# Performance work log

Hardware: AMD Instinct MI355X
Metric: run time of the kernel (lower is better)

The kernel has to match this reference:

```python
import jax, jax.numpy as jnp
import numpy as np

HEADS = 4
DIM_HEAD = 32
SCALE = DIM_HEAD ** (-0.5)


def setup_inputs() -> dict:
    key = jax.random.key(0)
    k1, k2, k3, k4 = jax.random.split(key, 4)
    dim = 256
    hidden = HEADS * DIM_HEAD  # 128
    x = jax.random.normal(k1, (8, dim, 48, 48), dtype=jnp.float32)
    w_qkv = jax.random.normal(k2, (3 * hidden, dim), dtype=jnp.float32) * (dim ** -0.5)
    w_out = jax.random.normal(k3, (dim, hidden), dtype=jnp.float32) * (hidden ** -0.5)
    b_out = jax.random.normal(k4, (dim,), dtype=jnp.float32) * 0.01
    return {"x": x, "w_qkv": w_qkv, "w_out": w_out, "b_out": b_out}


def reference(x, w_qkv, w_out, b_out):
    b, c, h, w = x.shape
    n = h * w
    xf = x.reshape(b, c, n)                                  # [b, c, n]
    # 1x1 Conv1d (no bias) == pointwise linear over channels
    qkv = jnp.einsum('oc,bcn->bon', w_qkv, xf)               # [b, 3*hidden, n]
    q, k, v = jnp.split(qkv, 3, axis=1)                      # each [b, hidden, n]
    def to_heads(t):
        return t.reshape(b, HEADS, DIM_HEAD, n)              # b h d n
    q, k, v = to_heads(q) * SCALE, to_heads(k), to_heads(v)
    sim = jnp.einsum('bhdi,bhdj->bhij', q, k)                # [b, h, n, n]
    attn = jax.nn.softmax(sim, axis=-1)                      # stable (max-subtracted)
    out = jnp.einsum('bhij,bhdj->bhid', attn, v)             # [b, h, n, d]
    # 'b h (x y) d -> b (h d) x y'
    out = out.transpose(0, 1, 3, 2).reshape(b, HEADS * DIM_HEAD, n)
    y = jnp.einsum('oc,bcn->bon', w_out, out) + b_out[None, :, None]
    return y.reshape(b, c, h, w)
```

## Files before the change

### kernel.cpp

```cpp
#include <hip/hip_runtime.h>
#include <math.h>

#define NB    8
#define CDIM  256
#define NN    2304
#define NH    4
#define DH    32
#define HIDC  128
#define OC3   384
#define SCALE_LOG2E 0.25503524964550864f
#define SEG   2359296
#define LSEG  73728
#define PPARTS 4
#define JCHUNK 576
#define NITER  18

typedef short  bf16x8 __attribute__((ext_vector_type(8)));
typedef float  f32x4  __attribute__((ext_vector_type(4)));

__device__ __forceinline__ unsigned short f2bf(float f) {
    union { float f; unsigned u; } a; a.f = f;
    unsigned r = a.u + 0x7fffu + ((a.u >> 16) & 1u);
    return (unsigned short)(r >> 16);
}

__device__ __forceinline__ unsigned pack_trunc(float lo, float hi) {
    union { float f; unsigned u; } a, b; a.f = lo; b.f = hi;
    return (b.u & 0xFFFF0000u) | (a.u >> 16);
}

__device__ __forceinline__ float bflo(unsigned u) {
    union { unsigned u; float f; } c; c.u = u << 16; return c.f;
}
__device__ __forceinline__ float bfhi(unsigned u) {
    union { unsigned u; float f; } c; c.u = u & 0xFFFF0000u; return c.f;
}

__global__ __launch_bounds__(256) void qkv_proj_kernel(
    const float* __restrict__ x, const float* __restrict__ w,
    unsigned short* __restrict__ qt, unsigned short* __restrict__ kt,
    unsigned short* __restrict__ vtT)
{
    __shared__ unsigned short As[128 * 40];
    __shared__ unsigned short Bs[128 * 40];
    const int Lb   = (int)blockIdx.x;
    const int xcd  = Lb & 7;
    const int t    = Lb >> 3;
    const int sel  = t % 3;
    const int gl   = t / 3;
    const int group = gl * 8 + xcd;
    const int nb   = group % 18;
    const int b    = group / 18;
    const int n0 = nb * 128;
    const int o0 = sel * 128;

    const int tid  = (int)threadIdx.x;
    const int wave = tid >> 6;
    const int lane = tid & 63;
    const int li   = lane & 15;
    const int g    = lane >> 4;
    const int wm = (wave & 1) * 64;
    const int wn = (wave >> 1) * 64;
    const float* xb = x + (size_t)b * CDIM * NN;

    const int aco = (tid & 7) * 4;
    const int aor = tid >> 3;
    const int n4  = (tid & 31) * 4;
    const int c4  = (tid >> 5) * 4;

    f32x4 acc[4][4];
#pragma unroll
    for (int i = 0; i < 4; ++i)
#pragma unroll
        for (int j = 0; j < 4; ++j) acc[i][j] = (f32x4){0.f, 0.f, 0.f, 0.f};

    float4 wv[4], xv[4];
#pragma unroll
    for (int r = 0; r < 4; ++r)
        wv[r] = *(const float4*)&w[(size_t)(o0 + aor + 32 * r) * CDIM + aco];
#pragma unroll
    for (int dd = 0; dd < 4; ++dd)
        xv[dd] = *(const float4*)&xb[(size_t)(c4 + dd) * NN + n0 + n4];

    for (int k0 = 0; k0 < CDIM; k0 += 32) {
        __syncthreads();
#pragma unroll
        for (int r = 0; r < 4; ++r) {
            uint2 pk;
            pk.x = (unsigned)f2bf(wv[r].x) | ((unsigned)f2bf(wv[r].y) << 16);
            pk.y = (unsigned)f2bf(wv[r].z) | ((unsigned)f2bf(wv[r].w) << 16);
            *(uint2*)&As[(aor + 32 * r) * 40 + aco] = pk;
        }
#pragma unroll
        for (int j = 0; j < 4; ++j) {
            uint2 pk;
            pk.x = (unsigned)f2bf(((const float*)&xv[0])[j])
                 | ((unsigned)f2bf(((const float*)&xv[1])[j]) << 16);
            pk.y = (unsigned)f2bf(((const float*)&xv[2])[j])
                 | ((unsigned)f2bf(((const float*)&xv[3])[j]) << 16);
            *(uint2*)&Bs[(n4 + j) * 40 + c4] = pk;
        }
        __syncthreads();

        const int kn = (k0 + 32 < CDIM) ? (k0 + 32) : k0;
#pragma unroll
        for (int r = 0; r < 4; ++r)
            wv[r] = *(const float4*)&w[(size_t)(o0 + aor + 32 * r) * CDIM + kn + aco];
#pragma unroll
        for (int dd = 0; dd < 4; ++dd)
            xv[dd] = *(const float4*)&xb[(size_t)(kn + c4 + dd) * NN + n0 + n4];

        bf16x8 af[4], bfr[4];
#pragma unroll
        for (int mt = 0; mt < 4; ++mt)
            af[mt] = *(const bf16x8*)&As[(wm + mt * 16 + li) * 40 + g * 8];
#pragma unroll
        for (int nt = 0; nt < 4; ++nt)
            bfr[nt] = *(const bf16x8*)&Bs[(wn + nt * 16 + li) * 40 + g * 8];
#pragma unroll
        for (int mt = 0; mt < 4; ++mt)
#pragma unroll
            for (int nt = 0; nt < 4; ++nt)
                acc[mt][nt] = __builtin_amdgcn_mfma_f32_16x16x32_bf16(
                    af[mt], bfr[nt], acc[mt][nt], 0, 0, 0);
    }

    if (sel < 2) {
        unsigned short* dst = (sel == 0) ? qt : kt;
        const float mul = (sel == 0) ? SCALE_LOG2E : 1.0f;
#pragma unroll
        for (int mt = 0; mt < 4; ++mt) {
            const int ob = o0 + wm + mt * 16 + g * 4;
            const int d0 = ob & 31;
            const int h  = (ob & 127) >> 5;
            const size_t bh = (size_t)(b * NH + h);
#pragma unroll
            for (int nt = 0; nt < 4; ++nt) {
                const int n = n0 + wn + nt * 16 + li;
                const f32x4 a = acc[mt][nt];
                uint2 pk;
                pk.x = (unsigned)f2bf(a[0] * mul) | ((unsigned)f2bf(a[1] * mul) << 16);
                pk.y = (unsigned)f2bf(a[2] * mul) | ((unsigned)f2bf(a[3] * mul) << 16);
                *(uint2*)&dst[(bh * NN + n) * DH + d0] = pk;
            }
        }
    } else {
#pragma unroll
        for (int mt = 0; mt < 4; ++mt) {
            const int ob = o0 + wm + mt * 16 + g * 4;
            const int d0 = ob & 31;
            const int h  = (ob & 127) >> 5;
            const size_t bh = (size_t)(b * NH + h);
#pragma unroll
            for (int nt = 0; nt < 4; ++nt) {
                const int n = n0 + wn + nt * 16 + li;
                const f32x4 a = acc[mt][nt];
#pragma unroll
                for (int r = 0; r < 4; ++r)
                    vtT[(bh * DH + d0 + r) * (size_t)NN + n] = f2bf(a[r]);
            }
        }
    }
}

__global__ __launch_bounds__(256) void attn_kernel(
    const unsigned short* __restrict__ qt, const unsigned short* __restrict__ kt,
    const unsigned short* __restrict__ vtT, unsigned short* __restrict__ Op,
    float* __restrict__ Lp)
{
    __shared__ unsigned short Pl[4][2][16 * 32];
    const int Lb  = (int)blockIdx.x;
    const int xcd = Lb & 7;
    const int t   = Lb >> 3;
    const int ib  = t % 18;
    const int grp = (t / 18) * 8 + xcd;
    const int bh  = grp >> 2;
    const int part = grp & 3;
    const int jbeg = part * JCHUNK;

    const int tid  = (int)threadIdx.x;
    const int wave = tid >> 6;
    const int lane = tid & 63;
    const int li   = lane & 15;
    const int g    = lane >> 4;
    const int i0   = ib * 128 + wave * 32;

    const unsigned short* qb = qt  + (size_t)bh * NN * DH;
    const unsigned short* kb = kt  + (size_t)bh * NN * DH;
    const unsigned short* vb = vtT + (size_t)bh * DH * NN;

    bf16x8 qfA = *(const bf16x8*)(qb + (size_t)(i0 + li) * DH + g * 8);
    bf16x8 qfB = *(const bf16x8*)(qb + (size_t)(i0 + 16 + li) * DH + g * 8);

    bf16x8 ones;
#pragma unroll
    for (int r = 0; r < 8; ++r) ones[r] = (short)0x3F80;

    f32x4 O0A = {0.f,0.f,0.f,0.f}, O1A = {0.f,0.f,0.f,0.f}, LsA = {0.f,0.f,0.f,0.f};
    f32x4 O0B = {0.f,0.f,0.f,0.f}, O1B = {0.f,0.f,0.f,0.f}, LsB = {0.f,0.f,0.f,0.f};
    unsigned short* plA = &Pl[wave][0][0];
    unsigned short* plB = &Pl[wave][1][0];
    const int sw  = li & 6;
    const int pw  = li * 32;
    const int wr0 = pw + ((g ^ sw) << 2);
    const int wr1 = pw + (((4 + g) ^ sw) << 2);
    const int rdo = pw + (((2 * g) ^ sw) << 2);

    const unsigned short* kp0 = kb + (size_t)(jbeg + li) * DH + g * 8;
    const unsigned short* kp1 = kp0 + 16 * DH;
    const unsigned short* vp0 = vb + (size_t)li * NN + jbeg + g * 8;
    const unsigned short* vp1 = vp0 + 16 * NN;

    bf16x8 kf0 = *(const bf16x8*)kp0;
    bf16x8 kf1 = *(const bf16x8*)kp1;
    bf16x8 vf0 = *(const bf16x8*)vp0;
    bf16x8 vf1 = *(const bf16x8*)vp1;

#pragma unroll 2
    for (int it = 0; it < NITER; ++it) {
        f32x4 z = {0.f, 0.f, 0.f, 0.f};
        f32x4 s0A = __builtin_amdgcn_mfma_f32_16x16x32_bf16(kf0, qfA, z, 0, 0, 0);
        f32x4 s0B = __builtin_amdgcn_mfma_f32_16x16x32_bf16(kf0, qfB, z, 0, 0, 0);
        f32x4 s1A = __builtin_amdgcn_mfma_f32_16x16x32_bf16(kf1, qfA, z, 0, 0, 0);
        f32x4 s1B = __builtin_amdgcn_mfma_f32_16x16x32_bf16(kf1, qfB, z, 0, 0, 0);

        kp0 += 32 * DH; kp1 += 32 * DH;
        kf0 = *(const bf16x8*)kp0;
        kf1 = *(const bf16x8*)kp1;

        float p0A[4], p1A[4], p0B[4], p1B[4];
#pragma unroll
        for (int r = 0; r < 4; ++r) {
            p0A[r] = __builtin_amdgcn_exp2f(s0A[r]);
            p1A[r] = __builtin_amdgcn_exp2f(s1A[r]);
            p0B[r] = __builtin_amdgcn_exp2f(s0B[r]);
            p1B[r] = __builtin_amdgcn_exp2f(s1B[r]);
        }

        uint2 wa, wb;
        wa.x = pack_trunc(p0A[0], p0A[1]);  wa.y = pack_trunc(p0A[2], p0A[3]);
        wb.x = pack_trunc(p1A[0], p1A[1]);  wb.y = pack_trunc(p1A[2], p1A[3]);
        *(uint2*)&plA[wr0] = wa;
        *(uint2*)&plA[wr1] = wb;
        wa.x = pack_trunc(p0B[0], p0B[1]);  wa.y = pack_trunc(p0B[2], p0B[3]);
        wb.x = pack_trunc(p1B[0], p1B[1]);  wb.y = pack_trunc(p1B[2], p1B[3]);
        *(uint2*)&plB[wr0] = wa;
        *(uint2*)&plB[wr1] = wb;

        bf16x8 pfA = *(const bf16x8*)&plA[rdo];
        bf16x8 pfB = *(const bf16x8*)&plB[rdo];

        O0A = __builtin_amdgcn_mfma_f32_16x16x32_bf16(vf0,  pfA, O0A, 0, 0, 0);
        O0B = __builtin_amdgcn_mfma_f32_16x16x32_bf16(vf0,  pfB, O0B, 0, 0, 0);
        O1A = __builtin_amdgcn_mfma_f32_16x16x32_bf16(vf1,  pfA, O1A, 0, 0, 0);
        O1B = __builtin_amdgcn_mfma_f32_16x16x32_bf16(vf1,  pfB, O1B, 0, 0, 0);
        LsA = __builtin_amdgcn_mfma_f32_16x16x32_bf16(ones, pfA, LsA, 0, 0, 0);
        LsB = __builtin_amdgcn_mfma_f32_16x16x32_bf16(ones, pfB, LsB, 0, 0, 0);

        vp0 += 32; vp1 += 32;
        vf0 = *(const bf16x8*)vp0;
        vf1 = *(const bf16x8*)vp1;
    }

    unsigned short* obA = Op + (size_t)part * SEG + (size_t)bh * DH * NN + i0 + li;
    unsigned short* obB = obA + 16;
#pragma unroll
    for (int r = 0; r < 4; ++r) {
        obA[(size_t)(4 * g + r)      * NN] = f2bf(O0A[r]);
        obA[(size_t)(16 + 4 * g + r) * NN] = f2bf(O1A[r]);
        obB[(size_t)(4 * g + r)      * NN] = f2bf(O0B[r]);
        obB[(size_t)(16 + 4 * g + r) * NN] = f2bf(O1B[r]);
    }
    if (g == 0) {
        Lp[(size_t)part * LSEG + (size_t)bh * NN + i0 + li]      = LsA[0];
        Lp[(size_t)part * LSEG + (size_t)bh * NN + i0 + 16 + li] = LsB[0];
    }
}

__global__ __launch_bounds__(256) void out_proj_kernel(
    const unsigned short* __restrict__ Op, const float* __restrict__ Lp,
    const float* __restrict__ w, const float* __restrict__ bias,
    float* __restrict__ y)
{
    __shared__ unsigned short As[128 * 40];
    __shared__ unsigned short Bs[128 * 40];
    __shared__ float Linv[4][128];
    const int Lb   = (int)blockIdx.x;
    const int xcd  = Lb & 7;
    const int t    = Lb >> 3;
    const int so_  = t % 2;
    const int gl   = t / 2;
    const int group = gl * 8 + xcd;
    const int nb   = group % 18;
    const int b    = group / 18;
    const int n0 = nb * 128;
    const int o0 = so_ * 128;

    const int tid  = (int)threadIdx.x;
    const int wave = tid >> 6;
    const int lane = tid & 63;
    const int li   = lane & 15;
    const int g    = lane >> 4;
    const int wm = (wave & 1) * 64;
    const int wn = (wave >> 1) * 64;

    const int aco = (tid & 7) * 4;
    const int aor = tid >> 3;
    const int n4  = (tid & 31) * 4;
    const int d4  = (tid >> 5) * 4;

    {
        const int h = tid >> 6, nb2 = tid & 63;
#pragma unroll
        for (int half = 0; half < 2; ++half) {
            const int n = nb2 + 64 * half;
            float s = 0.f;
#pragma unroll
            for (int p = 0; p < PPARTS; ++p)
                s += Lp[(size_t)p * LSEG + (size_t)(b * NH + h) * NN + n0 + n];
            Linv[h][n] = 1.0f / s;
        }
    }

    f32x4 acc[4][4];
#pragma unroll
    for (int i = 0; i < 4; ++i)
#pragma unroll
        for (int j = 0; j < 4; ++j) acc[i][j] = (f32x4){0.f, 0.f, 0.f, 0.f};

    float4 wv[4];
    uint2  ov[PPARTS][4];
#pragma unroll
    for (int r = 0; r < 4; ++r)
        wv[r] = *(const float4*)&w[(size_t)(o0 + aor + 32 * r) * HIDC + aco];
    {
        const size_t bh0 = (size_t)(b * NH);
#pragma unroll
        for (int p = 0; p < PPARTS; ++p)
#pragma unroll
            for (int dd = 0; dd < 4; ++dd)
                ov[p][dd] = *(const uint2*)&Op[(size_t)p * SEG
                              + (bh0 * DH + d4 + dd) * (size_t)NN + n0 + n4];
    }

    for (int k0 = 0; k0 < HIDC; k0 += 32) {
        __syncthreads();
#pragma unroll
        for (int r = 0; r < 4; ++r) {
            uint2 pk;
            pk.x = (unsigned)f2bf(wv[r].x) | ((unsigned)f2bf(wv[r].y) << 16);
            pk.y = (unsigned)f2bf(wv[r].z) | ((unsigned)f2bf(wv[r].w) << 16);
            *(uint2*)&As[(aor + 32 * r) * 40 + aco] = pk;
        }
        const int h = k0 >> 5;
        {
            float s[4][4];
#pragma unroll
            for (int dd = 0; dd < 4; ++dd)
#pragma unroll
                for (int j = 0; j < 4; ++j) s[dd][j] = 0.f;
#pragma unroll
            for (int p = 0; p < PPARTS; ++p) {
#pragma unroll
                for (int dd = 0; dd < 4; ++dd) {
                    const uint2 u = ov[p][dd];
                    s[dd][0] += bflo(u.x); s[dd][1] += bfhi(u.x);
                    s[dd][2] += bflo(u.y); s[dd][3] += bfhi(u.y);
                }
            }
#pragma unroll
            for (int j = 0; j < 4; ++j) {
                const float lv = Linv[h][n4 + j];
                uint2 pk;
                pk.x = (unsigned)f2bf(s[0][j] * lv) | ((unsigned)f2bf(s[1][j] * lv) << 16);
                pk.y = (unsigned)f2bf(s[2][j] * lv) | ((unsigned)f2bf(s[3][j] * lv) << 16);
                *(uint2*)&Bs[(n4 + j) * 40 + d4] = pk;
            }
        }
        __syncthreads();

        const int kn = (k0 + 32 < HIDC) ? (k0 + 32) : k0;
        const size_t bhn = (size_t)(b * NH + (kn >> 5));
#pragma unroll
        for (int r = 0; r < 4; ++r)
            wv[r] = *(const float4*)&w[(size_t)(o0 + aor + 32 * r) * HIDC + kn + aco];
#pragma unroll
        for (int p = 0; p < PPARTS; ++p)
#pragma unroll
            for (int dd = 0; dd < 4; ++dd)
                ov[p][dd] = *(const uint2*)&Op[(size_t)p * SEG
                              + (bhn * DH + d4 + dd) * (size_t)NN + n0 + n4];

        bf16x8 af[4], bfr[4];
#pragma unroll
        for (int mt = 0; mt < 4; ++mt)
            af[mt] = *(const bf16x8*)&As[(wm + mt * 16 + li) * 40 + g * 8];
#pragma unroll
        for (int nt = 0; nt < 4; ++nt)
            bfr[nt] = *(const bf16x8*)&Bs[(wn + nt * 16 + li) * 40 + g * 8];
#pragma unroll
        for (int mt = 0; mt < 4; ++mt)
#pragma unroll
            for (int nt = 0; nt < 4; ++nt)
                acc[mt][nt] = __builtin_amdgcn_mfma_f32_16x16x32_bf16(
                    af[mt], bfr[nt], acc[mt][nt], 0, 0, 0);
    }

#pragma unroll
    for (int mt = 0; mt < 4; ++mt) {
        const int ob = o0 + wm + mt * 16 + g * 4;
        const float b0 = bias[ob], b1 = bias[ob + 1], b2 = bias[ob + 2], b3 = bias[ob + 3];
#pragma unroll
        for (int nt = 0; nt < 4; ++nt) {
            const int n = n0 + wn + nt * 16 + li;
            const f32x4 a = acc[mt][nt];
            float* yb = y + ((size_t)(b * CDIM + ob)) * NN + n;
            yb[0]              = a[0] + b0;
            yb[(size_t)NN]     = a[1] + b1;
            yb[(size_t)2 * NN] = a[2] + b2;
            yb[(size_t)3 * NN] = a[3] + b3;
        }
    }
}

extern "C" void kernel_launch(void* const* d_in, const int* in_sizes, int n_in,
                              void* d_out, int out_size, void* d_ws, size_t ws_size,
                              hipStream_t stream)
{
    (void)in_sizes; (void)n_in; (void)out_size; (void)ws_size;
    const float* x     = (const float*)d_in[0];
    const float* w_qkv = (const float*)d_in[1];
    const float* w_out = (const float*)d_in[2];
    const float* b_out = (const float*)d_in[3];
    float* y = (float*)d_out;

    unsigned short* qt  = (unsigned short*)d_ws;
    unsigned short* kt  = qt + SEG;
    unsigned short* vtT = kt + SEG;
    unsigned short* Op  = vtT + SEG;
    float* Lp = (float*)(Op + (size_t)PPARTS * SEG);

    qkv_proj_kernel<<<dim3(432), 256, 0, stream>>>(x, w_qkv, qt, kt, vtT);

    attn_kernel<<<dim3(2304), 256, 0, stream>>>(qt, kt, vtT, Op, Lp);

    out_proj_kernel<<<dim3(288), 256, 0, stream>>>(Op, Lp, w_out, b_out, y);
}
```

Measured before the change: 165.4 us.

## Give each attention wave six query fragments and swizzle B tiles in shared memory

```diff
diff --git a/kernel.cpp b/kernel.cpp
--- a/kernel.cpp
+++ b/kernel.cpp
@@ -14,6 +14,7 @@
 #define PPARTS 4
 #define JCHUNK 576
 #define NITER  18
+#define NFRAG 6
 
 typedef short  bf16x8 __attribute__((ext_vector_type(8)));
 typedef float  f32x4  __attribute__((ext_vector_type(4)));
@@ -67,6 +68,9 @@
     const int aor = tid >> 3;
     const int n4  = (tid & 31) * 4;
     const int c4  = (tid >> 5) * 4;
+    const int l5   = tid & 31;
+    const int bkey = (l5 ^ (l5 >> 2)) & 3;
+    const int bsw  = ((((tid >> 6) ^ bkey) << 1) | ((tid >> 5) & 1)) << 2;
 
     f32x4 acc[4][4];
 #pragma unroll
@@ -98,7 +102,7 @@
                  | ((unsigned)f2bf(((const float*)&xv[1])[j]) << 16);
             pk.y = (unsigned)f2bf(((const float*)&xv[2])[j])
                  | ((unsigned)f2bf(((const float*)&xv[3])[j]) << 16);
-            *(uint2*)&Bs[(n4 + j) * 40 + c4] = pk;
+            *(uint2*)&Bs[(n4 + j) * 40 + bsw] = pk;
         }
         __syncthreads();
 
@@ -115,8 +119,11 @@
         for (int mt = 0; mt < 4; ++mt)
             af[mt] = *(const bf16x8*)&As[(wm + mt * 16 + li) * 40 + g * 8];
 #pragma unroll
-        for (int nt = 0; nt < 4; ++nt)
-            bfr[nt] = *(const bf16x8*)&Bs[(wn + nt * 16 + li) * 40 + g * 8];
+        for (int nt = 0; nt < 4; ++nt) {
+            const int rr = wn + nt * 16 + li;
+            const int rm = rr >> 2;
+            bfr[nt] = *(const bf16x8*)&Bs[rr * 40 + ((g ^ ((rm ^ (rm >> 2)) & 3)) << 3)];
+        }
 #pragma unroll
         for (int mt = 0; mt < 4; ++mt)
 #pragma unroll
@@ -168,12 +175,12 @@
     const unsigned short* __restrict__ vtT, unsigned short* __restrict__ Op,
     float* __restrict__ Lp)
 {
-    __shared__ unsigned short Pl[4][2][16 * 32];
+    __shared__ unsigned short Pl[4][NFRAG][512];
     const int Lb  = (int)blockIdx.x;
     const int xcd = Lb & 7;
     const int t   = Lb >> 3;
-    const int ib  = t % 18;
-    const int grp = (t / 18) * 8 + xcd;
+    const int ib  = t % NFRAG;
+    const int grp = (t / NFRAG) * 8 + xcd;
     const int bh  = grp >> 2;
     const int part = grp & 3;
     const int jbeg = part * JCHUNK;
@@ -183,23 +190,29 @@
     const int lane = tid & 63;
     const int li   = lane & 15;
     const int g    = lane >> 4;
-    const int i0   = ib * 128 + wave * 32;
+    const int i0   = ib * 384 + wave * 96;
 
     const unsigned short* qb = qt  + (size_t)bh * NN * DH;
     const unsigned short* kb = kt  + (size_t)bh * NN * DH;
     const unsigned short* vb = vtT + (size_t)bh * DH * NN;
 
-    bf16x8 qfA = *(const bf16x8*)(qb + (size_t)(i0 + li) * DH + g * 8);
-    bf16x8 qfB = *(const bf16x8*)(qb + (size_t)(i0 + 16 + li) * DH + g * 8);
+    bf16x8 qf[NFRAG];
+#pragma unroll
+    for (int f = 0; f < NFRAG; ++f)
+        qf[f] = *(const bf16x8*)(qb + (size_t)(i0 + f * 16 + li) * DH + g * 8);
 
     bf16x8 ones;
 #pragma unroll
     for (int r = 0; r < 8; ++r) ones[r] = (short)0x3F80;
 
-    f32x4 O0A = {0.f,0.f,0.f,0.f}, O1A = {0.f,0.f,0.f,0.f}, LsA = {0.f,0.f,0.f,0.f};
-    f32x4 O0B = {0.f,0.f,0.f,0.f}, O1B = {0.f,0.f,0.f,0.f}, LsB = {0.f,0.f,0.f,0.f};
-    unsigned short* plA = &Pl[wave][0][0];
-    unsigned short* plB = &Pl[wave][1][0];
+    f32x4 O0[NFRAG], O1[NFRAG], Ls[NFRAG];
+#pragma unroll
+    for (int f = 0; f < NFRAG; ++f) {
+        O0[f] = (f32x4){0.f, 0.f, 0.f, 0.f};
+        O1[f] = (f32x4){0.f, 0.f, 0.f, 0.f};
+        Ls[f] = (f32x4){0.f, 0.f, 0.f, 0.f};
+    }
+
     const int sw  = li & 6;
     const int pw  = li * 32;
     const int wr0 = pw + ((g ^ sw) << 2);
@@ -216,64 +229,76 @@
     bf16x8 vf0 = *(const bf16x8*)vp0;
     bf16x8 vf1 = *(const bf16x8*)vp1;
 
-#pragma unroll 2
+#pragma unroll 1
     for (int it = 0; it < NITER; ++it) {
-        f32x4 z = {0.f, 0.f, 0.f, 0.f};
-        f32x4 s0A = __builtin_amdgcn_mfma_f32_16x16x32_bf16(kf0, qfA, z, 0, 0, 0);
-        f32x4 s0B = __builtin_amdgcn_mfma_f32_16x16x32_bf16(kf0, qfB, z, 0, 0, 0);
-        f32x4 s1A = __builtin_amdgcn_mfma_f32_16x16x32_bf16(kf1, qfA, z, 0, 0, 0);
-        f32x4 s1B = __builtin_amdgcn_mfma_f32_16x16x32_bf16(kf1, qfB, z, 0, 0, 0);
+        const f32x4 z = {0.f, 0.f, 0.f, 0.f};
+        f32x4 s0[NFRAG], s1[NFRAG];
+#pragma unroll
+        for (int f = 0; f < NFRAG; ++f)
+            s0[f] = __builtin_amdgcn_mfma_f32_16x16x32_bf16(kf0, qf[f], z, 0, 0, 0);
+#pragma unroll
+        for (int f = 0; f < NFRAG; ++f)
+            s1[f] = __builtin_amdgcn_mfma_f32_16x16x32_bf16(kf1, qf[f], z, 0, 0, 0);
 
         kp0 += 32 * DH; kp1 += 32 * DH;
         kf0 = *(const bf16x8*)kp0;
         kf1 = *(const bf16x8*)kp1;
 
-        float p0A[4], p1A[4], p0B[4], p1B[4];
-#pragma unroll
-        for (int r = 0; r < 4; ++r) {
-            p0A[r] = __builtin_amdgcn_exp2f(s0A[r]);
-            p1A[r] = __builtin_amdgcn_exp2f(s1A[r]);
-            p0B[r] = __builtin_amdgcn_exp2f(s0B[r]);
-            p1B[r] = __builtin_amdgcn_exp2f(s1B[r]);
-        }
-
-        uint2 wa, wb;
-        wa.x = pack_trunc(p0A[0], p0A[1]);  wa.y = pack_trunc(p0A[2], p0A[3]);
-        wb.x = pack_trunc(p1A[0], p1A[1]);  wb.y = pack_trunc(p1A[2], p1A[3]);
-        *(uint2*)&plA[wr0] = wa;
-        *(uint2*)&plA[wr1] = wb;
-        wa.x = pack_trunc(p0B[0], p0B[1]);  wa.y = pack_trunc(p0B[2], p0B[3]);
-        wb.x = pack_trunc(p1B[0], p1B[1]);  wb.y = pack_trunc(p1B[2], p1B[3]);
-        *(uint2*)&plB[wr0] = wa;
-        *(uint2*)&plB[wr1] = wb;
-
-        bf16x8 pfA = *(const bf16x8*)&plA[rdo];
-        bf16x8 pfB = *(const bf16x8*)&plB[rdo];
-
-        O0A = __builtin_amdgcn_mfma_f32_16x16x32_bf16(vf0,  pfA, O0A, 0, 0, 0);
-        O0B = __builtin_amdgcn_mfma_f32_16x16x32_bf16(vf0,  pfB, O0B, 0, 0, 0);
-        O1A = __builtin_amdgcn_mfma_f32_16x16x32_bf16(vf1,  pfA, O1A, 0, 0, 0);
-        O1B = __builtin_amdgcn_mfma_f32_16x16x32_bf16(vf1,  pfB, O1B, 0, 0, 0);
-        LsA = __builtin_amdgcn_mfma_f32_16x16x32_bf16(ones, pfA, LsA, 0, 0, 0);
-        LsB = __builtin_amdgcn_mfma_f32_16x16x32_bf16(ones, pfB, LsB, 0, 0, 0);
+        float p0[NFRAG][4], p1[NFRAG][4];
+#pragma unroll
+        for (int f = 0; f < NFRAG; ++f)
+#pragma unroll
+            for (int r = 0; r < 4; ++r) {
+                p0[f][r] = __builtin_amdgcn_exp2f(s0[f][r]);
+                p1[f][r] = __builtin_amdgcn_exp2f(s1[f][r]);
+            }
+
+#pragma unroll
+        for (int f = 0; f < NFRAG; ++f) {
+            uint2 wa, wb;
+            wa.x = pack_trunc(p0[f][0], p0[f][1]);
+            wa.y = pack_trunc(p0[f][2], p0[f][3]);
+            wb.x = pack_trunc(p1[f][0], p1[f][1]);
+            wb.y = pack_trunc(p1[f][2], p1[f][3]);
+            *(uint2*)&Pl[wave][f][wr0] = wa;
+            *(uint2*)&Pl[wave][f][wr1] = wb;
+        }
+
+        bf16x8 pf[NFRAG];
+#pragma unroll
+        for (int f = 0; f < NFRAG; ++f)
+            pf[f] = *(const bf16x8*)&Pl[wave][f][rdo];
+
+#pragma unroll
+        for (int f = 0; f < NFRAG; ++f)
+            O0[f] = __builtin_amdgcn_mfma_f32_16x16x32_bf16(vf0,  pf[f], O0[f], 0, 0, 0);
+#pragma unroll
+        for (int f = 0; f < NFRAG; ++f)
+            O1[f] = __builtin_amdgcn_mfma_f32_16x16x32_bf16(vf1,  pf[f], O1[f], 0, 0, 0);
+#pragma unroll
+        for (int f = 0; f < NFRAG; ++f)
+            Ls[f] = __builtin_amdgcn_mfma_f32_16x16x32_bf16(ones, pf[f], Ls[f], 0, 0, 0);
 
         vp0 += 32; vp1 += 32;
         vf0 = *(const bf16x8*)vp0;
         vf1 = *(const bf16x8*)vp1;
     }
 
-    unsigned short* obA = Op + (size_t)part * SEG + (size_t)bh * DH * NN + i0 + li;
-    unsigned short* obB = obA + 16;
-#pragma unroll
-    for (int r = 0; r < 4; ++r) {
-        obA[(size_t)(4 * g + r)      * NN] = f2bf(O0A[r]);
-        obA[(size_t)(16 + 4 * g + r) * NN] = f2bf(O1A[r]);
-        obB[(size_t)(4 * g + r)      * NN] = f2bf(O0B[r]);
-        obB[(size_t)(16 + 4 * g + r) * NN] = f2bf(O1B[r]);
+    unsigned short* ob = Op + (size_t)part * SEG + (size_t)bh * DH * NN + i0 + li;
+#pragma unroll
+    for (int f = 0; f < NFRAG; ++f) {
+        unsigned short* obf = ob + f * 16;
+#pragma unroll
+        for (int r = 0; r < 4; ++r) {
+            obf[(size_t)(4 * g + r)      * NN] = f2bf(O0[f][r]);
+            obf[(size_t)(16 + 4 * g + r) * NN] = f2bf(O1[f][r]);
+        }
     }
     if (g == 0) {
-        Lp[(size_t)part * LSEG + (size_t)bh * NN + i0 + li]      = LsA[0];
-        Lp[(size_t)part * LSEG + (size_t)bh * NN + i0 + 16 + li] = LsB[0];
+        float* lpb = Lp + (size_t)part * LSEG + (size_t)bh * NN + i0 + li;
+#pragma unroll
+        for (int f = 0; f < NFRAG; ++f)
+            lpb[f * 16] = Ls[f][0];
     }
 }
 
@@ -308,6 +333,9 @@
     const int aor = tid >> 3;
     const int n4  = (tid & 31) * 4;
     const int d4  = (tid >> 5) * 4;
+    const int l5   = tid & 31;
+    const int bkey = (l5 ^ (l5 >> 2)) & 3;
+    const int bsw  = ((((tid >> 6) ^ bkey) << 1) | ((tid >> 5) & 1)) << 2;
 
     {
         const int h = tid >> 6, nb2 = tid & 63;
@@ -374,7 +402,7 @@
                 uint2 pk;
                 pk.x = (unsigned)f2bf(s[0][j] * lv) | ((unsigned)f2bf(s[1][j] * lv) << 16);
                 pk.y = (unsigned)f2bf(s[2][j] * lv) | ((unsigned)f2bf(s[3][j] * lv) << 16);
-                *(uint2*)&Bs[(n4 + j) * 40 + d4] = pk;
+                *(uint2*)&Bs[(n4 + j) * 40 + bsw] = pk;
             }
         }
         __syncthreads();
@@ -396,8 +424,11 @@
         for (int mt = 0; mt < 4; ++mt)
             af[mt] = *(const bf16x8*)&As[(wm + mt * 16 + li) * 40 + g * 8];
 #pragma unroll
-        for (int nt = 0; nt < 4; ++nt)
-            bfr[nt] = *(const bf16x8*)&Bs[(wn + nt * 16 + li) * 40 + g * 8];
+        for (int nt = 0; nt < 4; ++nt) {
+            const int rr = wn + nt * 16 + li;
+            const int rm = rr >> 2;
+            bfr[nt] = *(const bf16x8*)&Bs[rr * 40 + ((g ^ ((rm ^ (rm >> 2)) & 3)) << 3)];
+        }
 #pragma unroll
         for (int mt = 0; mt < 4; ++mt)
 #pragma unroll
@@ -442,7 +473,7 @@
 
     qkv_proj_kernel<<<dim3(432), 256, 0, stream>>>(x, w_qkv, qt, kt, vtT);
 
-    attn_kernel<<<dim3(2304), 256, 0, stream>>>(qt, kt, vtT, Op, Lp);
+    attn_kernel<<<dim3(768), 256, 0, stream>>>(qt, kt, vtT, Op, Lp);
 
     out_proj_kernel<<<dim3(288), 256, 0, stream>>>(Op, Lp, w_out, b_out, y);
 }
```

Result: faster. 135.3 us, median of 2 (-18.2%).
